# Optimization experiments

Measured on AMD Instinct MI355X. Metric: run time of the kernel, lower is better.

Reference implementation:

```python
import jax, jax.numpy as jnp
import numpy as np

B, S, HID = 2, 2048, 2048
NH = 16
Q_LORA, KV_LORA = 1024, 512
NOPE, ROPE, VD = 128, 64, 128
QK = NOPE + ROPE  # 192
EPS = 1e-6
THETA = 10000.0


def rms_norm(x, w, eps=EPS):
    x32 = x.astype(jnp.float32)
    var = jnp.mean(x32 * x32, axis=-1, keepdims=True)
    return (w * (x32 * jax.lax.rsqrt(var + eps))).astype(x.dtype)


def rotate_half(x):
    h = x.shape[-1] // 2
    return jnp.concatenate([-x[..., h:], x[..., :h]], axis=-1)


def setup_inputs() -> dict:
    key = jax.random.key(0)
    ks = jax.random.split(key, 8)
    hidden_states = jax.random.normal(ks[0], (B, S, HID), dtype=jnp.float32)
    attention_mask = jnp.zeros((B, 1, 1, S), dtype=jnp.float32)
    # RoPE tables (true rotary values)
    inv_freq = 1.0 / (THETA ** (np.arange(0, ROPE, 2, dtype=np.float32) / ROPE))
    pos = np.arange(S, dtype=np.float32)
    freqs = np.outer(pos, inv_freq)  # [S, ROPE/2]
    emb = np.concatenate([freqs, freqs], axis=-1)  # [S, ROPE]
    cos = jnp.asarray(np.cos(emb), dtype=jnp.float32)
    sin = jnp.asarray(np.sin(emb), dtype=jnp.float32)
    # Parameters, stored as [in, out] so y = x @ W
    sd = lambda fan_in: 1.0 / np.sqrt(fan_in)
    w_q_down = jax.random.normal(ks[1], (HID, Q_LORA), dtype=jnp.float32) * sd(HID)
    w_q_up = jax.random.normal(ks[2], (Q_LORA, NH * QK), dtype=jnp.float32) * sd(Q_LORA)
    w_kv_down = jax.random.normal(ks[3], (HID, KV_LORA + ROPE), dtype=jnp.float32) * sd(HID)
    w_kv_up = jax.random.normal(ks[4], (KV_LORA, NH * (NOPE + VD)), dtype=jnp.float32) * sd(KV_LORA)
    w_o = jax.random.normal(ks[5], (NH * VD, HID), dtype=jnp.float32) * sd(NH * VD)
    q_norm_w = jnp.ones((Q_LORA,), dtype=jnp.float32)
    kv_norm_w = jnp.ones((KV_LORA,), dtype=jnp.float32)
    return dict(hidden_states=hidden_states, attention_mask=attention_mask,
                cos=cos, sin=sin, w_q_down=w_q_down, w_q_up=w_q_up,
                w_kv_down=w_kv_down, w_kv_up=w_kv_up, w_o=w_o,
                q_norm_w=q_norm_w, kv_norm_w=kv_norm_w)


def reference(hidden_states, attention_mask, cos, sin,
              w_q_down, w_q_up, w_kv_down, w_kv_up, w_o,
              q_norm_w, kv_norm_w):
    b, s, _ = hidden_states.shape
    # --- Q path: down-proj -> RMSNorm -> up-proj ---
    q = rms_norm(hidden_states @ w_q_down, q_norm_w) @ w_q_up  # [b,s,NH*QK]
    q = q.reshape(b, s, NH, QK).transpose(0, 2, 1, 3)          # [b,h,s,QK]
    q_nope, q_rope = q[..., :NOPE], q[..., NOPE:]
    # --- KV path: down-proj -> split latent / rope key -> up-proj ---
    kv = hidden_states @ w_kv_down                              # [b,s,KV_LORA+ROPE]
    kv_latent, k_rope = kv[..., :KV_LORA], kv[..., KV_LORA:]
    kv_up = rms_norm(kv_latent, kv_norm_w) @ w_kv_up            # [b,s,NH*(NOPE+VD)]
    kv_up = kv_up.reshape(b, s, NH, NOPE + VD).transpose(0, 2, 1, 3)
    k_nope, v = kv_up[..., :NOPE], kv_up[..., NOPE:]            # [b,h,s,*]
    k_rope = k_rope[:, None, :, :]                              # [b,1,s,ROPE] (broadcast over heads)
    # --- partial RoPE ---
    c = cos[None, None, :, :]
    sn = sin[None, None, :, :]
    q_rope = q_rope * c + rotate_half(q_rope) * sn
    k_rope = k_rope * c + rotate_half(k_rope) * sn
    q_final = jnp.concatenate([q_nope, q_rope], axis=-1)        # [b,h,s,QK]
    k_final = jnp.concatenate([k_nope, jnp.broadcast_to(k_rope, (b, NH, s, ROPE))], axis=-1)
    # --- SDPA (non-causal, additive mask) ---
    scale = 1.0 / jnp.sqrt(jnp.asarray(QK, dtype=jnp.float32))
    scores = jnp.einsum('bhqd,bhkd->bhqk', q_final, k_final) * scale
    scores = scores + attention_mask                            # [b,1,1,s] broadcast
    probs = jax.nn.softmax(scores.astype(jnp.float32), axis=-1).astype(q_final.dtype)
    attn = jnp.einsum('bhqk,bhkd->bhqd', probs, v)              # [b,h,s,VD]
    attn = attn.transpose(0, 2, 1, 3).reshape(b, s, NH * VD)
    return attn @ w_o
```

## Files before the change

### kernel.cpp

```cpp
#include <hip/hip_runtime.h>
#include <hip/hip_bf16.h>

typedef unsigned short u16;
typedef unsigned int u32;
typedef short s16x8 __attribute__((ext_vector_type(8)));
typedef float f32x4 __attribute__((ext_vector_type(4)));
typedef float f32x2 __attribute__((ext_vector_type(2)));

__device__ __forceinline__ float bf2f(u16 u) {
    union { u32 i; float f; } v; v.i = ((u32)u) << 16; return v.f;
}
__device__ __forceinline__ u16 f2bf(float f) {
    union { float f; u32 i; } v; v.f = f;
    u32 i = v.i;
    u32 r = (i + 0x7FFFu + ((i >> 16) & 1u)) >> 16;
    return (u16)r;
}

__device__ __forceinline__ void gl2lds16(const u16* g, u16* l) {
    __builtin_amdgcn_global_load_lds(
        (const __attribute__((address_space(1))) u32*)g,
        (__attribute__((address_space(3))) u32*)l, 16, 0, 0);
}

__global__ __launch_bounds__(256) void cvt_f32_bf16(
    const float* __restrict__ in, u16* __restrict__ out, long long n2)
{
    long long i = (long long)blockIdx.x * 256 + threadIdx.x;
    if (i < n2) {
        f32x2 v = *(const f32x2*)(in + i * 2);
        u32 p = (u32)f2bf(v[0]) | ((u32)f2bf(v[1]) << 16);
        *(u32*)(out + i * 2) = p;
    }
}

__global__ __launch_bounds__(256) void transpose_f32_bf16(
    const float* __restrict__ in, u16* __restrict__ out, int R, int C)
{
    __shared__ u16 t[32][33];
    int tx = threadIdx.x & 31, ty = threadIdx.x >> 5;
    int c0 = blockIdx.x * 32, r0 = blockIdx.y * 32;
    #pragma unroll
    for (int i = 0; i < 32; i += 8)
        t[ty + i][tx] = f2bf(in[(size_t)(r0 + ty + i) * C + c0 + tx]);
    __syncthreads();
    #pragma unroll
    for (int i = 0; i < 32; i += 8)
        out[(size_t)(c0 + ty + i) * R + r0 + tx] = t[tx][ty + i];
}

__global__ __launch_bounds__(256) void transpose_v(
    const u16* __restrict__ kvup, u16* __restrict__ vt)
{
    __shared__ u16 t[32][33];
    int tx = threadIdx.x & 31, ty = threadIdx.x >> 5;
    int s0 = blockIdx.x * 32, v0 = blockIdx.y * 32;
    int b = blockIdx.z >> 4, h = blockIdx.z & 15;
    #pragma unroll
    for (int i = 0; i < 32; i += 8)
        t[ty + i][tx] = kvup[(size_t)(b * 2048 + s0 + ty + i) * 4096 + h * 256 + 128 + v0 + tx];
    __syncthreads();
    #pragma unroll
    for (int i = 0; i < 32; i += 8)
        vt[((size_t)(b * 16 + h) * 128 + v0 + ty + i) * 2048 + s0 + tx] = t[tx][ty + i];
}

__global__ __launch_bounds__(256) void gemm_bf16(
    const u16* __restrict__ A, const u16* __restrict__ Bt, u16* __restrict__ C,
    int M, int N, int K)
{
    __shared__ u16 As[64][40];
    __shared__ u16 Bs[64][40];

    const int tid  = threadIdx.x;
    const int wave = tid >> 6, lane = tid & 63;
    const int quad = lane >> 4, l16 = lane & 15;
    const int m0 = blockIdx.y * 64, n0 = blockIdx.x * 64;
    const int wm = (wave >> 1) * 32, wn = (wave & 1) * 32;

    const int srow = tid >> 2;
    const int koff = (tid & 3) * 8;

    f32x4 acc00 = {0.f,0.f,0.f,0.f};
    f32x4 acc01 = {0.f,0.f,0.f,0.f};
    f32x4 acc10 = {0.f,0.f,0.f,0.f};
    f32x4 acc11 = {0.f,0.f,0.f,0.f};

    for (int k0 = 0; k0 < K; k0 += 32) {
        *(s16x8*)&As[srow][koff] = *(const s16x8*)&A[(size_t)(m0 + srow) * K + k0 + koff];
        *(s16x8*)&Bs[srow][koff] = *(const s16x8*)&Bt[(size_t)(n0 + srow) * K + k0 + koff];
        __syncthreads();
        s16x8 a0 = *(const s16x8*)&As[wm + l16][quad * 8];
        s16x8 a1 = *(const s16x8*)&As[wm + 16 + l16][quad * 8];
        s16x8 b0 = *(const s16x8*)&Bs[wn + l16][quad * 8];
        s16x8 b1 = *(const s16x8*)&Bs[wn + 16 + l16][quad * 8];
        acc00 = __builtin_amdgcn_mfma_f32_16x16x32_bf16(a0, b0, acc00, 0, 0, 0);
        acc01 = __builtin_amdgcn_mfma_f32_16x16x32_bf16(a0, b1, acc01, 0, 0, 0);
        acc10 = __builtin_amdgcn_mfma_f32_16x16x32_bf16(a1, b0, acc10, 0, 0, 0);
        acc11 = __builtin_amdgcn_mfma_f32_16x16x32_bf16(a1, b1, acc11, 0, 0, 0);
        __syncthreads();
    }

    #pragma unroll
    for (int r = 0; r < 4; ++r) {
        int row0 = m0 + wm + quad * 4 + r;
        int col0 = n0 + wn + l16;
        C[(size_t)row0 * N + col0]             = f2bf(acc00[r]);
        C[(size_t)row0 * N + col0 + 16]        = f2bf(acc01[r]);
        C[(size_t)(row0 + 16) * N + col0]      = f2bf(acc10[r]);
        C[(size_t)(row0 + 16) * N + col0 + 16] = f2bf(acc11[r]);
    }
}

template <typename OUT>
__global__ __launch_bounds__(256) void gemm128(
    const u16* __restrict__ A, const u16* __restrict__ Bt, OUT* __restrict__ C,
    int M, int N, int K)
{
    __shared__ u16 As[128 * 32];
    __shared__ u16 Bs[128 * 32];

    const int tid  = threadIdx.x;
    const int wave = tid >> 6, lane = tid & 63;
    const int quad = lane >> 4, l16 = lane & 15;
    const int m0 = blockIdx.y * 128, n0 = blockIdx.x * 128;
    const int wm = (wave >> 1) * 64, wn = (wave & 1) * 64;

    const int srow = lane >> 2, soct = (lane & 3) * 8;

    f32x4 acc[4][4];
    #pragma unroll
    for (int i = 0; i < 4; ++i)
        #pragma unroll
        for (int j = 0; j < 4; ++j) acc[i][j] = (f32x4){0.f,0.f,0.f,0.f};

    for (int k0 = 0; k0 < K; k0 += 32) {
        #pragma unroll
        for (int op = 0; op < 2; ++op) {
            int g = wave * 2 + op;
            gl2lds16(&A[(size_t)(m0 + g * 16 + srow) * K + k0 + soct], &As[g * 512]);
            gl2lds16(&Bt[(size_t)(n0 + g * 16 + srow) * K + k0 + soct], &Bs[g * 512]);
        }
        __syncthreads();
        s16x8 af[4], bf[4];
        #pragma unroll
        for (int i = 0; i < 4; ++i) {
            af[i] = *(const s16x8*)&As[(wm + i * 16 + l16) * 32 + quad * 8];
            bf[i] = *(const s16x8*)&Bs[(wn + i * 16 + l16) * 32 + quad * 8];
        }
        #pragma unroll
        for (int i = 0; i < 4; ++i)
            #pragma unroll
            for (int j = 0; j < 4; ++j)
                acc[i][j] = __builtin_amdgcn_mfma_f32_16x16x32_bf16(af[i], bf[j], acc[i][j], 0, 0, 0);
        __syncthreads();
    }

    #pragma unroll
    for (int i = 0; i < 4; ++i) {
        #pragma unroll
        for (int j = 0; j < 4; ++j) {
            #pragma unroll
            for (int r = 0; r < 4; ++r) {
                int row = m0 + wm + i * 16 + quad * 4 + r;
                int col = n0 + wn + j * 16 + l16;
                if constexpr (sizeof(OUT) == 2)
                    C[(size_t)row * N + col] = f2bf(acc[i][j][r]);
                else
                    C[(size_t)row * N + col] = acc[i][j][r];
            }
        }
    }
}

__global__ __launch_bounds__(256) void rmsnorm_kernel(
    const u16* __restrict__ in, const float* __restrict__ w, u16* __restrict__ out,
    int len, int istride, int ostride)
{
    const int row = blockIdx.x, tid = threadIdx.x;
    const u16* x = in + (size_t)row * istride;
    float ss = 0.f;
    for (int i = tid; i < len; i += 256) { float v = bf2f(x[i]); ss += v * v; }
    #pragma unroll
    for (int off = 32; off >= 1; off >>= 1) ss += __shfl_xor(ss, off, 64);
    __shared__ float wsum[4];
    if ((tid & 63) == 0) wsum[tid >> 6] = ss;
    __syncthreads();
    float tot = wsum[0] + wsum[1] + wsum[2] + wsum[3];
    float inv = 1.0f / sqrtf(tot / (float)len + 1e-6f);
    for (int i = tid; i < len; i += 256) {
        float v = bf2f(x[i]);
        out[(size_t)row * ostride + i] = f2bf(v * inv * w[i]);
    }
}

__global__ __launch_bounds__(256) void rope_kernel(
    u16* __restrict__ qb, const u16* __restrict__ kvb, u16* __restrict__ krot,
    const float* __restrict__ cosb, const float* __restrict__ sinb)
{
    const int row = blockIdx.x;
    const int s = row & 2047;
    const int lane = threadIdx.x & 63, wave = threadIdx.x >> 6;
    const float c  = cosb[s * 64 + lane];
    const float sn = sinb[s * 64 + lane];
    for (int seg = wave; seg < 17; seg += 4) {
        const u16* pin; u16* pout;
        if (seg < 16) { pout = qb + (size_t)row * 3072 + seg * 192 + 128; pin = pout; }
        else          { pin = kvb + (size_t)row * 576 + 512; pout = krot + (size_t)row * 64; }
        float x  = bf2f(pin[lane]);
        float xp = bf2f(pin[lane ^ 32]);
        float rot = (lane < 32) ? -xp : xp;
        pout[lane] = f2bf(x * c + rot * sn);
    }
}

__global__ __launch_bounds__(256, 2) void attn_mfma3(
    const u16* __restrict__ qb,
    const u16* __restrict__ kvup,
    const u16* __restrict__ krot,
    const u16* __restrict__ vt,
    const float* __restrict__ mask,
    u16* __restrict__ attnb)
{
    __shared__ u16 Ks[64][200];
    __shared__ u16 Vs[128][72];
    __shared__ u16 Ps[128][72];

    const int tid  = threadIdx.x;
    const int wave = tid >> 6, lane = tid & 63;
    const int quad = lane >> 4, l16 = lane & 15;
    const int qt = blockIdx.x, h = blockIdx.y, b = blockIdx.z;
    const int row0 = b * 2048 + qt * 128;
    const int qw = wave * 16;
    const float scale = 0.07216878364870323f;

    s16x8 onesf;
    #pragma unroll
    for (int j = 0; j < 8; ++j) onesf[j] = (short)0x3F80;

    s16x8 qf[2][6];
    #pragma unroll
    for (int s = 0; s < 2; ++s)
        #pragma unroll
        for (int kc = 0; kc < 6; ++kc)
            qf[s][kc] = *(const s16x8*)&qb[(size_t)(row0 + s * 64 + qw + l16) * 3072
                                           + h * 192 + kc * 32 + quad * 8];

    float m = -__builtin_inff();
    f32x4 l[2] = {(f32x4){0.f,0.f,0.f,0.f}, (f32x4){0.f,0.f,0.f,0.f}};
    f32x4 O[2][8];
    #pragma unroll
    for (int s = 0; s < 2; ++s)
        #pragma unroll
        for (int vi = 0; vi < 8; ++vi) O[s][vi] = (f32x4){0.f,0.f,0.f,0.f};

    const u16* vtb = vt + ((size_t)(b * 16 + h) * 128) * 2048;

    for (int kt = 0; kt < 32; ++kt) {
        const int krow0 = b * 2048 + kt * 64;
        __syncthreads();
        #pragma unroll
        for (int i = 0; i < 6; ++i) {
            int idx = tid + i * 256;
            int r = idx / 24, c = (idx % 24) * 8;
            const u16* src = (c < 128)
                ? &kvup[(size_t)(krow0 + r) * 4096 + h * 256 + c]
                : &krot[(size_t)(krow0 + r) * 64 + (c - 128)];
            *(s16x8*)&Ks[r][c] = *(const s16x8*)src;
        }
        #pragma unroll
        for (int i = 0; i < 4; ++i) {
            int idx = tid + i * 256;
            int r = idx >> 3, c8 = (idx & 7) * 8;
            *(s16x8*)&Vs[r][c8] = *(const s16x8*)&vtb[(size_t)r * 2048 + kt * 64 + c8];
        }
        __syncthreads();

        f32x4 S[2][4];
        #pragma unroll
        for (int s = 0; s < 2; ++s)
            #pragma unroll
            for (int ct = 0; ct < 4; ++ct) S[s][ct] = (f32x4){0.f,0.f,0.f,0.f};
        #pragma unroll
        for (int kc = 0; kc < 6; ++kc) {
            #pragma unroll
            for (int ct = 0; ct < 4; ++ct) {
                s16x8 bf = *(const s16x8*)&Ks[ct * 16 + l16][kc * 32 + quad * 8];
                S[0][ct] = __builtin_amdgcn_mfma_f32_16x16x32_bf16(qf[0][kc], bf, S[0][ct], 0, 0, 0);
                S[1][ct] = __builtin_amdgcn_mfma_f32_16x16x32_bf16(qf[1][kc], bf, S[1][ct], 0, 0, 0);
            }
        }
        #pragma unroll
        for (int ct = 0; ct < 4; ++ct) {
            float mv = mask[b * 2048 + kt * 64 + ct * 16 + l16];
            #pragma unroll
            for (int s = 0; s < 2; ++s)
                #pragma unroll
                for (int r = 0; r < 4; ++r) S[s][ct][r] = S[s][ct][r] * scale + mv;
        }
        float tm = S[0][0][0];
        #pragma unroll
        for (int s = 0; s < 2; ++s)
            #pragma unroll
            for (int ct = 0; ct < 4; ++ct)
                #pragma unroll
                for (int r = 0; r < 4; ++r) tm = fmaxf(tm, S[s][ct][r]);
        #pragma unroll
        for (int off = 1; off < 64; off <<= 1)
            tm = fmaxf(tm, __shfl_xor(tm, off, 64));
        float mn = fmaxf(m, tm);
        float alpha = __expf(m - mn);
        m = mn;
        #pragma unroll
        for (int s = 0; s < 2; ++s)
            #pragma unroll
            for (int ct = 0; ct < 4; ++ct)
                #pragma unroll
                for (int r = 0; r < 4; ++r)
                    Ps[s * 64 + qw + quad * 4 + r][ct * 16 + l16] = f2bf(__expf(S[s][ct][r] - m));
        #pragma unroll
        for (int s = 0; s < 2; ++s) {
            l[s] *= alpha;
            #pragma unroll
            for (int vi = 0; vi < 8; ++vi) O[s][vi] *= alpha;
        }
        #pragma unroll
        for (int kc = 0; kc < 2; ++kc) {
            s16x8 a0 = *(const s16x8*)&Ps[qw + l16][kc * 32 + quad * 8];
            s16x8 a1 = *(const s16x8*)&Ps[64 + qw + l16][kc * 32 + quad * 8];
            #pragma unroll
            for (int vi = 0; vi < 8; ++vi) {
                s16x8 bf = *(const s16x8*)&Vs[vi * 16 + l16][kc * 32 + quad * 8];
                O[0][vi] = __builtin_amdgcn_mfma_f32_16x16x32_bf16(a0, bf, O[0][vi], 0, 0, 0);
                O[1][vi] = __builtin_amdgcn_mfma_f32_16x16x32_bf16(a1, bf, O[1][vi], 0, 0, 0);
            }
            l[0] = __builtin_amdgcn_mfma_f32_16x16x32_bf16(a0, onesf, l[0], 0, 0, 0);
            l[1] = __builtin_amdgcn_mfma_f32_16x16x32_bf16(a1, onesf, l[1], 0, 0, 0);
        }
    }

    #pragma unroll
    for (int s = 0; s < 2; ++s) {
        f32x4 linv;
        #pragma unroll
        for (int r = 0; r < 4; ++r) linv[r] = 1.0f / l[s][r];
        #pragma unroll
        for (int vi = 0; vi < 8; ++vi) {
            #pragma unroll
            for (int r = 0; r < 4; ++r) {
                int q_ = row0 + s * 64 + qw + quad * 4 + r;
                attnb[(size_t)q_ * 2048 + h * 128 + vi * 16 + l16] = f2bf(O[s][vi][r] * linv[r]);
            }
        }
    }
}

extern "C" void kernel_launch(void* const* d_in, const int* in_sizes, int n_in,
                              void* d_out, int out_size, void* d_ws, size_t ws_size,
                              hipStream_t stream)
{
    const float* hidden = (const float*)d_in[0];
    const float* mask   = (const float*)d_in[1];
    const float* cosb   = (const float*)d_in[2];
    const float* sinb   = (const float*)d_in[3];
    const float* w_qd   = (const float*)d_in[4];
    const float* w_qu   = (const float*)d_in[5];
    const float* w_kvd  = (const float*)d_in[6];
    const float* w_kvu  = (const float*)d_in[7];
    const float* w_o    = (const float*)d_in[8];
    const float* qnw    = (const float*)d_in[9];
    const float* kvnw   = (const float*)d_in[10];
    float* out = (float*)d_out;

    u16* ws = (u16*)d_ws;
    u16* qbuf   = ws + 0;
    u16* wt_qd  = ws + 0;
    u16* kvup   = ws + 12582912;
    u16* hid_bf = ws + 12582912;
    u16* wt_kvd = ws + 20971520;
    u16* attnb  = ws + 29360128;
    u16* qd     = ws + 29360128;
    u16* wt_qu  = ws + 33554432;
    u16* kvb    = ws + 37748736;
    u16* wt_o   = ws + 37748736;
    u16* kvn    = ws + 40108032;
    u16* wt_kvu = ws + 42205184;
    u16* krot   = ws + 44302336;
    u16* vt     = ws + 44564480;

    {
        long long n2 = (long long)4096 * 2048 / 2;
        cvt_f32_bf16<<<(int)((n2 + 255) / 256), 256, 0, stream>>>(hidden, hid_bf, n2);
    }

    transpose_f32_bf16<<<dim3(32, 64), 256, 0, stream>>>(w_qd, wt_qd, 2048, 1024);
    gemm128<u16><<<dim3(8, 32), 256, 0, stream>>>(hid_bf, wt_qd, qd, 4096, 1024, 2048);
    rmsnorm_kernel<<<4096, 256, 0, stream>>>(qd, qnw, qd, 1024, 1024, 1024);
    transpose_f32_bf16<<<dim3(96, 32), 256, 0, stream>>>(w_qu, wt_qu, 1024, 3072);
    gemm128<u16><<<dim3(24, 32), 256, 0, stream>>>(qd, wt_qu, qbuf, 4096, 3072, 1024);

    transpose_f32_bf16<<<dim3(18, 64), 256, 0, stream>>>(w_kvd, wt_kvd, 2048, 576);
    gemm_bf16<<<dim3(9, 64), 256, 0, stream>>>(hid_bf, wt_kvd, kvb, 4096, 576, 2048);
    rmsnorm_kernel<<<4096, 256, 0, stream>>>(kvb, kvnw, kvn, 512, 576, 512);
    transpose_f32_bf16<<<dim3(128, 16), 256, 0, stream>>>(w_kvu, wt_kvu, 512, 4096);
    gemm128<u16><<<dim3(32, 32), 256, 0, stream>>>(kvn, wt_kvu, kvup, 4096, 4096, 512);

    transpose_v<<<dim3(64, 4, 32), 256, 0, stream>>>(kvup, vt);

    rope_kernel<<<4096, 256, 0, stream>>>(qbuf, kvb, krot, cosb, sinb);
    transpose_f32_bf16<<<dim3(64, 64), 256, 0, stream>>>(w_o, wt_o, 2048, 2048);

    attn_mfma3<<<dim3(16, 16, 2), 256, 0, stream>>>(qbuf, kvup, krot, vt, mask, attnb);

    gemm128<float><<<dim3(16, 32), 256, 0, stream>>>(attnb, wt_o, out, 4096, 2048, 2048);
}
```

Before: 519.4 us.

## Prefetch K via registers and double-buffer V with async LDS loads in attention

The attention kernel now loads the next K tile into registers while the current tile is being used, instead of loading it synchronously between barriers. V is double-buffered in shared memory and filled with global_load_lds, using an XOR swizzle to avoid bank conflicts. Softmax uses exp2 with the log2(e) factor folded into the scale and mask, and s_setprio raises priority around the MFMA blocks. The cost is more registers and shared memory, which could limit occupancy under the two-blocks-per-CU launch bound.

```diff
diff --git a/kernel.cpp b/kernel.cpp
--- a/kernel.cpp
+++ b/kernel.cpp
@@ -214,7 +214,7 @@
     }
 }
 
-__global__ __launch_bounds__(256, 2) void attn_mfma3(
+__global__ __launch_bounds__(256, 2) void attn_mfma4(
     const u16* __restrict__ qb,
     const u16* __restrict__ kvup,
     const u16* __restrict__ krot,
@@ -222,9 +222,9 @@
     const float* __restrict__ mask,
     u16* __restrict__ attnb)
 {
-    __shared__ u16 Ks[64][200];
-    __shared__ u16 Vs[128][72];
-    __shared__ u16 Ps[128][72];
+    __shared__ u16 Ks[64 * 200];
+    __shared__ u16 Ps[128 * 72];
+    __shared__ u16 Vd[2][128 * 64];
 
     const int tid  = threadIdx.x;
     const int wave = tid >> 6, lane = tid & 63;
@@ -232,7 +232,9 @@
     const int qt = blockIdx.x, h = blockIdx.y, b = blockIdx.z;
     const int row0 = b * 2048 + qt * 128;
     const int qw = wave * 16;
-    const float scale = 0.07216878364870323f;
+    const float scale2 = 0.10411610f;
+    const float l2e    = 1.4426950408889634f;
+    const int swz = (l16 & 7) << 3;
 
     s16x8 onesf;
     #pragma unroll
@@ -246,6 +248,35 @@
             qf[s][kc] = *(const s16x8*)&qb[(size_t)(row0 + s * 64 + qw + l16) * 3072
                                            + h * 192 + kc * 32 + quad * 8];
 
+    const u16* pk[6]; int offk[6], stepk[6];
+    #pragma unroll
+    for (int i = 0; i < 6; ++i) {
+        int idx = tid + i * 256;
+        int r = idx / 24, c = (idx % 24) * 8;
+        offk[i] = r * 200 + c;
+        if (c < 128) { pk[i] = kvup + (size_t)(b * 2048 + r) * 4096 + h * 256 + c; stepk[i] = 64 * 4096; }
+        else         { pk[i] = krot + (size_t)(b * 2048 + r) * 64 + (c - 128);     stepk[i] = 64 * 64;   }
+    }
+
+    const u16* vtb = vt + (size_t)(b * 16 + h) * 128 * 2048;
+    const u16* pv[4];
+    #pragma unroll
+    for (int i = 0; i < 4; ++i) {
+        int widx = i * 4 + wave;
+        int r = widx * 8 + (lane >> 3);
+        int u = (lane & 7) ^ (lane >> 3);
+        pv[i] = vtb + (size_t)r * 2048 + u * 8;
+    }
+
+    s16x8 kreg[6];
+    #pragma unroll
+    for (int i = 0; i < 6; ++i) { kreg[i] = *(const s16x8*)pk[i]; pk[i] += stepk[i]; }
+    #pragma unroll
+    for (int i = 0; i < 4; ++i) {
+        gl2lds16(pv[i], &Vd[0][(i * 4 + wave) * 512]);
+        pv[i] += 64;
+    }
+
     float m = -__builtin_inff();
     f32x4 l[2] = {(f32x4){0.f,0.f,0.f,0.f}, (f32x4){0.f,0.f,0.f,0.f}};
     f32x4 O[2][8];
@@ -254,50 +285,50 @@
         #pragma unroll
         for (int vi = 0; vi < 8; ++vi) O[s][vi] = (f32x4){0.f,0.f,0.f,0.f};
 
-    const u16* vtb = vt + ((size_t)(b * 16 + h) * 128) * 2048;
-
     for (int kt = 0; kt < 32; ++kt) {
-        const int krow0 = b * 2048 + kt * 64;
-        __syncthreads();
-        #pragma unroll
-        for (int i = 0; i < 6; ++i) {
-            int idx = tid + i * 256;
-            int r = idx / 24, c = (idx % 24) * 8;
-            const u16* src = (c < 128)
-                ? &kvup[(size_t)(krow0 + r) * 4096 + h * 256 + c]
-                : &krot[(size_t)(krow0 + r) * 64 + (c - 128)];
-            *(s16x8*)&Ks[r][c] = *(const s16x8*)src;
-        }
-        #pragma unroll
-        for (int i = 0; i < 4; ++i) {
-            int idx = tid + i * 256;
-            int r = idx >> 3, c8 = (idx & 7) * 8;
-            *(s16x8*)&Vs[r][c8] = *(const s16x8*)&vtb[(size_t)r * 2048 + kt * 64 + c8];
-        }
-        __syncthreads();
+        __syncthreads();
+        #pragma unroll
+        for (int i = 0; i < 6; ++i) *(s16x8*)&Ks[offk[i]] = kreg[i];
+        __syncthreads();
+
+        if (kt < 31) {
+            #pragma unroll
+            for (int i = 0; i < 6; ++i) { kreg[i] = *(const s16x8*)pk[i]; pk[i] += stepk[i]; }
+            #pragma unroll
+            for (int i = 0; i < 4; ++i) {
+                gl2lds16(pv[i], &Vd[(kt + 1) & 1][(i * 4 + wave) * 512]);
+                pv[i] += 64;
+            }
+        }
+        float mv4[4];
+        #pragma unroll
+        for (int ct = 0; ct < 4; ++ct)
+            mv4[ct] = mask[b * 2048 + kt * 64 + ct * 16 + l16] * l2e;
 
         f32x4 S[2][4];
         #pragma unroll
         for (int s = 0; s < 2; ++s)
             #pragma unroll
             for (int ct = 0; ct < 4; ++ct) S[s][ct] = (f32x4){0.f,0.f,0.f,0.f};
+        __builtin_amdgcn_s_setprio(1);
         #pragma unroll
         for (int kc = 0; kc < 6; ++kc) {
             #pragma unroll
             for (int ct = 0; ct < 4; ++ct) {
-                s16x8 bf = *(const s16x8*)&Ks[ct * 16 + l16][kc * 32 + quad * 8];
-                S[0][ct] = __builtin_amdgcn_mfma_f32_16x16x32_bf16(qf[0][kc], bf, S[0][ct], 0, 0, 0);
-                S[1][ct] = __builtin_amdgcn_mfma_f32_16x16x32_bf16(qf[1][kc], bf, S[1][ct], 0, 0, 0);
+                s16x8 bfr = *(const s16x8*)&Ks[(ct * 16 + l16) * 200 + kc * 32 + quad * 8];
+                S[0][ct] = __builtin_amdgcn_mfma_f32_16x16x32_bf16(qf[0][kc], bfr, S[0][ct], 0, 0, 0);
+                S[1][ct] = __builtin_amdgcn_mfma_f32_16x16x32_bf16(qf[1][kc], bfr, S[1][ct], 0, 0, 0);
             }
         }
-        #pragma unroll
-        for (int ct = 0; ct < 4; ++ct) {
-            float mv = mask[b * 2048 + kt * 64 + ct * 16 + l16];
+        __builtin_amdgcn_s_setprio(0);
+
+        #pragma unroll
+        for (int ct = 0; ct < 4; ++ct)
             #pragma unroll
             for (int s = 0; s < 2; ++s)
                 #pragma unroll
-                for (int r = 0; r < 4; ++r) S[s][ct][r] = S[s][ct][r] * scale + mv;
-        }
+                for (int r = 0; r < 4; ++r) S[s][ct][r] = S[s][ct][r] * scale2 + mv4[ct];
+
         float tm = S[0][0][0];
         #pragma unroll
         for (int s = 0; s < 2; ++s)
@@ -309,34 +340,43 @@
         for (int off = 1; off < 64; off <<= 1)
             tm = fmaxf(tm, __shfl_xor(tm, off, 64));
         float mn = fmaxf(m, tm);
-        float alpha = __expf(m - mn);
+        float alpha = exp2f(m - mn);
         m = mn;
+
         #pragma unroll
         for (int s = 0; s < 2; ++s)
             #pragma unroll
             for (int ct = 0; ct < 4; ++ct)
                 #pragma unroll
                 for (int r = 0; r < 4; ++r)
-                    Ps[s * 64 + qw + quad * 4 + r][ct * 16 + l16] = f2bf(__expf(S[s][ct][r] - m));
+                    Ps[(s * 64 + qw + quad * 4 + r) * 72 + ct * 16 + l16]
+                        = f2bf(exp2f(S[s][ct][r] - m));
+
         #pragma unroll
         for (int s = 0; s < 2; ++s) {
             l[s] *= alpha;
             #pragma unroll
             for (int vi = 0; vi < 8; ++vi) O[s][vi] *= alpha;
         }
+
+        const u16* Vb = Vd[kt & 1];
+        __builtin_amdgcn_s_setprio(1);
         #pragma unroll
         for (int kc = 0; kc < 2; ++kc) {
-            s16x8 a0 = *(const s16x8*)&Ps[qw + l16][kc * 32 + quad * 8];
-            s16x8 a1 = *(const s16x8*)&Ps[64 + qw + l16][kc * 32 + quad * 8];
+            s16x8 a0 = *(const s16x8*)&Ps[(qw + l16) * 72 + kc * 32 + quad * 8];
+            s16x8 a1 = *(const s16x8*)&Ps[(64 + qw + l16) * 72 + kc * 32 + quad * 8];
             #pragma unroll
             for (int vi = 0; vi < 8; ++vi) {
-                s16x8 bf = *(const s16x8*)&Vs[vi * 16 + l16][kc * 32 + quad * 8];
-                O[0][vi] = __builtin_amdgcn_mfma_f32_16x16x32_bf16(a0, bf, O[0][vi], 0, 0, 0);
-                O[1][vi] = __builtin_amdgcn_mfma_f32_16x16x32_bf16(a1, bf, O[1][vi], 0, 0, 0);
+                int rowv = vi * 16 + l16;
+                int col  = kc * 32 + quad * 8;
+                s16x8 bfr = *(const s16x8*)&Vb[rowv * 64 + (col ^ swz)];
+                O[0][vi] = __builtin_amdgcn_mfma_f32_16x16x32_bf16(a0, bfr, O[0][vi], 0, 0, 0);
+                O[1][vi] = __builtin_amdgcn_mfma_f32_16x16x32_bf16(a1, bfr, O[1][vi], 0, 0, 0);
             }
             l[0] = __builtin_amdgcn_mfma_f32_16x16x32_bf16(a0, onesf, l[0], 0, 0, 0);
             l[1] = __builtin_amdgcn_mfma_f32_16x16x32_bf16(a1, onesf, l[1], 0, 0, 0);
         }
+        __builtin_amdgcn_s_setprio(0);
     }
 
     #pragma unroll
@@ -410,7 +450,7 @@
     rope_kernel<<<4096, 256, 0, stream>>>(qbuf, kvb, krot, cosb, sinb);
     transpose_f32_bf16<<<dim3(64, 64), 256, 0, stream>>>(w_o, wt_o, 2048, 2048);
 
-    attn_mfma3<<<dim3(16, 16, 2), 256, 0, stream>>>(qbuf, kvup, krot, vt, mask, attnb);
+    attn_mfma4<<<dim3(16, 16, 2), 256, 0, stream>>>(qbuf, kvup, krot, vt, mask, attnb);
 
     gemm128<float><<<dim3(16, 32), 256, 0, stream>>>(attnb, wt_o, out, 4096, 2048, 2048);
 }
```

Measured after the change: 515.2 us. About the same (-0.8%).
